# Optimization experiments

Measured on AMD Instinct MI355X. Metric: run time of the kernel, lower is better.

Reference implementation:

```python
import jax, jax.numpy as jnp
import numpy as np


def _pairwise_smooth_l1_sum(x):
    # x: [N, D]. All N^2 ordered pairs (i, j), including i == j (diff = 0),
    # matching torch's full index_select over [i for i ... for j ...].
    d = x[:, None, :] - x[None, :, :]            # [N, N, D]
    ad = jnp.abs(d)
    # SmoothL1 with beta = 1 (torch default): 0.5*d^2 if |d| < 1 else |d| - 0.5
    sl1 = jnp.where(ad < 1.0, 0.5 * d * d, ad - 0.5)
    return jnp.sum(sl1, axis=-1).reshape(-1)     # [N*N]


def setup_inputs() -> dict:
    key = jax.random.key(0)
    k1, k2 = jax.random.split(key)
    N, D = 512, 512
    teacher = jax.random.normal(k1, (N, D), dtype=jnp.float32)
    student = jax.random.normal(k2, (N, D), dtype=jnp.float32)
    return {"teacher": teacher, "student": student}


def reference(teacher, student):
    teacher_l2s = _pairwise_smooth_l1_sum(teacher)
    teacher_l2s = teacher_l2s / jnp.mean(teacher_l2s)
    student_l2s = _pairwise_smooth_l1_sum(student)
    student_l2s = student_l2s / jnp.mean(student_l2s)
    return jnp.sum(jnp.abs(teacher_l2s - student_l2s))
```

## Files before the change

kernel.cpp:

```cpp
#include <hip/hip_runtime.h>

#define N 512
#define D 512
#define TILE 32
#define DC 64
#define PAD 68

__device__ __forceinline__ void sl1(float& acc, float x, float y) {
    float d  = x - y;
    float ad = fabsf(d);
    float m  = fminf(ad, 1.0f);
    acc = fmaf(m, fmaf(2.0f, ad, -m), acc);
}

__global__ __launch_bounds__(64) void zero_kernel(float* sums, float* out) {
    if (threadIdx.x == 0) { sums[0] = 0.0f; sums[1] = 0.0f; out[0] = 0.0f; }
}

__global__ __launch_bounds__(256) void pair_sums_kernel(
    const float* __restrict__ Tm, const float* __restrict__ Sm,
    float* __restrict__ P, float* __restrict__ sums)
{
    const int mat = blockIdx.z;
    const float* __restrict__ X = mat ? Sm : Tm;
    float* __restrict__ Pm = P + (size_t)mat * (N * N);

    __shared__ float Xi[TILE][PAD];
    __shared__ float Xj[TILE][PAD];

    const int i0 = blockIdx.y * TILE;
    const int j0 = blockIdx.x * TILE;
    const int t  = threadIdx.x;
    const int tx = t & 15;
    const int ty = t >> 4;

    float a00 = 0.f, a01 = 0.f, a10 = 0.f, a11 = 0.f;

    for (int dc = 0; dc < D; dc += DC) {
        __syncthreads();
        #pragma unroll
        for (int k = 0; k < 2; ++k) {
            int idx = t + k * 256;
            int row = idx >> 4;
            int c4  = (idx & 15) * 4;
            *(float4*)&Xi[row][c4] = *(const float4*)&X[(size_t)(i0 + row) * D + dc + c4];
            *(float4*)&Xj[row][c4] = *(const float4*)&X[(size_t)(j0 + row) * D + dc + c4];
        }
        __syncthreads();
        #pragma unroll 4
        for (int d4 = 0; d4 < DC / 4; ++d4) {
            float4 p0 = *(const float4*)&Xi[ty][d4 * 4];
            float4 p1 = *(const float4*)&Xi[ty + 16][d4 * 4];
            float4 q0 = *(const float4*)&Xj[tx][d4 * 4];
            float4 q1 = *(const float4*)&Xj[tx + 16][d4 * 4];
            sl1(a00, p0.x, q0.x); sl1(a00, p0.y, q0.y); sl1(a00, p0.z, q0.z); sl1(a00, p0.w, q0.w);
            sl1(a01, p0.x, q1.x); sl1(a01, p0.y, q1.y); sl1(a01, p0.z, q1.z); sl1(a01, p0.w, q1.w);
            sl1(a10, p1.x, q0.x); sl1(a10, p1.y, q0.y); sl1(a10, p1.z, q0.z); sl1(a10, p1.w, q0.w);
            sl1(a11, p1.x, q1.x); sl1(a11, p1.y, q1.y); sl1(a11, p1.z, q1.z); sl1(a11, p1.w, q1.w);
        }
    }

    float s00 = 0.5f * a00, s01 = 0.5f * a01, s10 = 0.5f * a10, s11 = 0.5f * a11;
    Pm[(size_t)(i0 + ty     ) * N + (j0 + tx     )] = s00;
    Pm[(size_t)(i0 + ty     ) * N + (j0 + tx + 16)] = s01;
    Pm[(size_t)(i0 + ty + 16) * N + (j0 + tx     )] = s10;
    Pm[(size_t)(i0 + ty + 16) * N + (j0 + tx + 16)] = s11;

    float bs = s00 + s01 + s10 + s11;
    #pragma unroll
    for (int off = 32; off > 0; off >>= 1) bs += __shfl_down(bs, off, 64);
    __shared__ float wpart[4];
    if ((t & 63) == 0) wpart[t >> 6] = bs;
    __syncthreads();
    if (t == 0) atomicAdd(&sums[mat], wpart[0] + wpart[1] + wpart[2] + wpart[3]);
}

__global__ __launch_bounds__(256) void final_kernel(
    const float* __restrict__ P, const float* __restrict__ sums, float* __restrict__ out)
{
    const float NN = (float)(N * N);
    const float cT = NN / sums[0];
    const float cS = NN / sums[1];
    float local = 0.0f;
    for (int p = blockIdx.x * 256 + threadIdx.x; p < N * N; p += gridDim.x * 256) {
        local += fabsf(P[p] * cT - P[N * N + p] * cS);
    }
    #pragma unroll
    for (int off = 32; off > 0; off >>= 1) local += __shfl_down(local, off, 64);
    __shared__ float wpart[4];
    if ((threadIdx.x & 63) == 0) wpart[threadIdx.x >> 6] = local;
    __syncthreads();
    if (threadIdx.x == 0) atomicAdd(out, wpart[0] + wpart[1] + wpart[2] + wpart[3]);
}

extern "C" void kernel_launch(void* const* d_in, const int* in_sizes, int n_in,
                              void* d_out, int out_size, void* d_ws, size_t ws_size,
                              hipStream_t stream) {
    const float* teacher = (const float*)d_in[0];
    const float* student = (const float*)d_in[1];
    float* out  = (float*)d_out;
    float* P    = (float*)d_ws;
    float* sums = P + 2 * (size_t)N * N;

    zero_kernel<<<1, 64, 0, stream>>>(sums, out);
    dim3 grid(N / TILE, N / TILE, 2);
    pair_sums_kernel<<<grid, 256, 0, stream>>>(teacher, student, P, sums);
    final_kernel<<<128, 256, 0, stream>>>(P, sums, out);
}
```

Measured before the change: 100.8 us.

## Exploit pair symmetry with upper-triangle tiles and split-D atomic accumulation

The pair kernel now computes only upper-triangular 32x32 tiles (136 instead of 256) and splits the feature dimension into 8 slices, one per block. Each block atomically adds its partial sums into a pre-zeroed workspace. The final kernel reads only the upper triangle with float4 loads and doubles the total, with the mean sums rescaled to match. This roughly halves the arithmetic and raises parallelism, at the cost of global float atomics, a full-workspace memset each call, and a possible change in float summation order.

```diff
diff --git a/kernel.cpp b/kernel.cpp
--- a/kernel.cpp
+++ b/kernel.cpp
@@ -4,7 +4,10 @@
 #define D 512
 #define TILE 32
 #define DC 64
-#define PAD 68
+#define PITCH 68
+#define NT 16
+#define NTILES 136
+#define NSLICE 8
 
 __device__ __forceinline__ void sl1(float& acc, float x, float y) {
     float d  = x - y;
@@ -13,11 +16,7 @@
     acc = fmaf(m, fmaf(2.0f, ad, -m), acc);
 }
 
-__global__ __launch_bounds__(64) void zero_kernel(float* sums, float* out) {
-    if (threadIdx.x == 0) { sums[0] = 0.0f; sums[1] = 0.0f; out[0] = 0.0f; }
-}
-
-__global__ __launch_bounds__(256) void pair_sums_kernel(
+__global__ __launch_bounds__(256, 8) void pair_sums_kernel(
     const float* __restrict__ Tm, const float* __restrict__ Sm,
     float* __restrict__ P, float* __restrict__ sums)
 {
@@ -25,48 +24,53 @@
     const float* __restrict__ X = mat ? Sm : Tm;
     float* __restrict__ Pm = P + (size_t)mat * (N * N);
 
-    __shared__ float Xi[TILE][PAD];
-    __shared__ float Xj[TILE][PAD];
+    int rem = blockIdx.x, ti = 0;
+    while (rem >= NT - ti) { rem -= NT - ti; ++ti; }
+    const int tj = ti + rem;
+    const int i0 = ti * TILE, j0 = tj * TILE;
+    const int d0 = blockIdx.y * DC;
 
-    const int i0 = blockIdx.y * TILE;
-    const int j0 = blockIdx.x * TILE;
+    __shared__ float Xi[TILE][PITCH];
+    __shared__ float Xj[TILE][PITCH];
+
     const int t  = threadIdx.x;
     const int tx = t & 15;
     const int ty = t >> 4;
 
+    #pragma unroll
+    for (int kk = 0; kk < 2; ++kk) {
+        int idx = t + kk * 256;
+        int row = idx >> 4;
+        int c4  = (idx & 15) * 4;
+        *(float4*)&Xi[row][c4] = *(const float4*)&X[(size_t)(i0 + row) * D + d0 + c4];
+        *(float4*)&Xj[row][c4] = *(const float4*)&X[(size_t)(j0 + row) * D + d0 + c4];
+    }
+    __syncthreads();
+
     float a00 = 0.f, a01 = 0.f, a10 = 0.f, a11 = 0.f;
-
-    for (int dc = 0; dc < D; dc += DC) {
-        __syncthreads();
-        #pragma unroll
-        for (int k = 0; k < 2; ++k) {
-            int idx = t + k * 256;
-            int row = idx >> 4;
-            int c4  = (idx & 15) * 4;
-            *(float4*)&Xi[row][c4] = *(const float4*)&X[(size_t)(i0 + row) * D + dc + c4];
-            *(float4*)&Xj[row][c4] = *(const float4*)&X[(size_t)(j0 + row) * D + dc + c4];
-        }
-        __syncthreads();
-        #pragma unroll 4
-        for (int d4 = 0; d4 < DC / 4; ++d4) {
-            float4 p0 = *(const float4*)&Xi[ty][d4 * 4];
-            float4 p1 = *(const float4*)&Xi[ty + 16][d4 * 4];
-            float4 q0 = *(const float4*)&Xj[tx][d4 * 4];
-            float4 q1 = *(const float4*)&Xj[tx + 16][d4 * 4];
-            sl1(a00, p0.x, q0.x); sl1(a00, p0.y, q0.y); sl1(a00, p0.z, q0.z); sl1(a00, p0.w, q0.w);
-            sl1(a01, p0.x, q1.x); sl1(a01, p0.y, q1.y); sl1(a01, p0.z, q1.z); sl1(a01, p0.w, q1.w);
-            sl1(a10, p1.x, q0.x); sl1(a10, p1.y, q0.y); sl1(a10, p1.z, q0.z); sl1(a10, p1.w, q0.w);
-            sl1(a11, p1.x, q1.x); sl1(a11, p1.y, q1.y); sl1(a11, p1.z, q1.z); sl1(a11, p1.w, q1.w);
-        }
+    #pragma unroll 4
+    for (int d4 = 0; d4 < DC / 4; ++d4) {
+        float4 p0 = *(const float4*)&Xi[ty][d4 * 4];
+        float4 p1 = *(const float4*)&Xi[ty + 16][d4 * 4];
+        float4 q0 = *(const float4*)&Xj[tx][d4 * 4];
+        float4 q1 = *(const float4*)&Xj[tx + 16][d4 * 4];
+        sl1(a00, p0.x, q0.x); sl1(a00, p0.y, q0.y); sl1(a00, p0.z, q0.z); sl1(a00, p0.w, q0.w);
+        sl1(a01, p0.x, q1.x); sl1(a01, p0.y, q1.y); sl1(a01, p0.z, q1.z); sl1(a01, p0.w, q1.w);
+        sl1(a10, p1.x, q0.x); sl1(a10, p1.y, q0.y); sl1(a10, p1.z, q0.z); sl1(a10, p1.w, q0.w);
+        sl1(a11, p1.x, q1.x); sl1(a11, p1.y, q1.y); sl1(a11, p1.z, q1.z); sl1(a11, p1.w, q1.w);
     }
 
-    float s00 = 0.5f * a00, s01 = 0.5f * a01, s10 = 0.5f * a10, s11 = 0.5f * a11;
-    Pm[(size_t)(i0 + ty     ) * N + (j0 + tx     )] = s00;
-    Pm[(size_t)(i0 + ty     ) * N + (j0 + tx + 16)] = s01;
-    Pm[(size_t)(i0 + ty + 16) * N + (j0 + tx     )] = s10;
-    Pm[(size_t)(i0 + ty + 16) * N + (j0 + tx + 16)] = s11;
+    const bool diag = (ti == tj);
+    const bool w00 = !diag || (ty <= tx);
+    const bool w10 = !diag;
+    const float s00 = 0.5f * a00, s01 = 0.5f * a01, s10 = 0.5f * a10, s11 = 0.5f * a11;
 
-    float bs = s00 + s01 + s10 + s11;
+    float bs = 0.f;
+    if (w00) { atomicAdd(&Pm[(i0 + ty     ) * N + (j0 + tx     )], s00); bs += s00; }
+              { atomicAdd(&Pm[(i0 + ty     ) * N + (j0 + tx + 16)], s01); bs += s01; }
+    if (w10) { atomicAdd(&Pm[(i0 + ty + 16) * N + (j0 + tx     )], s10); bs += s10; }
+    if (w00) { atomicAdd(&Pm[(i0 + ty + 16) * N + (j0 + tx + 16)], s11); bs += s11; }
+
     #pragma unroll
     for (int off = 32; off > 0; off >>= 1) bs += __shfl_down(bs, off, 64);
     __shared__ float wpart[4];
@@ -78,19 +82,28 @@
 __global__ __launch_bounds__(256) void final_kernel(
     const float* __restrict__ P, const float* __restrict__ sums, float* __restrict__ out)
 {
-    const float NN = (float)(N * N);
-    const float cT = NN / sums[0];
-    const float cS = NN / sums[1];
+    const float NN = (float)N * (float)N;
+    const float cT = NN / (2.0f * sums[0]);
+    const float cS = NN / (2.0f * sums[1]);
     float local = 0.0f;
-    for (int p = blockIdx.x * 256 + threadIdx.x; p < N * N; p += gridDim.x * 256) {
-        local += fabsf(P[p] * cT - P[N * N + p] * cS);
+    const int nvec = N * N / 4;
+    for (int v = blockIdx.x * 256 + threadIdx.x; v < nvec; v += gridDim.x * 256) {
+        int i  = v >> 7;
+        int jb = (v & 127) * 4;
+        if (jb + 3 < i) continue;
+        float4 tq = ((const float4*)P)[v];
+        float4 sq = ((const float4*)(P + (size_t)N * N))[v];
+        if (jb + 0 >= i) local += fabsf(tq.x * cT - sq.x * cS);
+        if (jb + 1 >= i) local += fabsf(tq.y * cT - sq.y * cS);
+        if (jb + 2 >= i) local += fabsf(tq.z * cT - sq.z * cS);
+        if (jb + 3 >= i) local += fabsf(tq.w * cT - sq.w * cS);
     }
     #pragma unroll
     for (int off = 32; off > 0; off >>= 1) local += __shfl_down(local, off, 64);
     __shared__ float wpart[4];
     if ((threadIdx.x & 63) == 0) wpart[threadIdx.x >> 6] = local;
     __syncthreads();
-    if (threadIdx.x == 0) atomicAdd(out, wpart[0] + wpart[1] + wpart[2] + wpart[3]);
+    if (threadIdx.x == 0) atomicAdd(out, 2.0f * (wpart[0] + wpart[1] + wpart[2] + wpart[3]));
 }
 
 extern "C" void kernel_launch(void* const* d_in, const int* in_sizes, int n_in,
@@ -102,8 +115,10 @@
     float* P    = (float*)d_ws;
     float* sums = P + 2 * (size_t)N * N;
 
-    zero_kernel<<<1, 64, 0, stream>>>(sums, out);
-    dim3 grid(N / TILE, N / TILE, 2);
+    hipMemsetAsync(d_ws, 0, (2 * (size_t)N * N + 2) * sizeof(float), stream);
+    hipMemsetAsync(d_out, 0, sizeof(float), stream);
+
+    dim3 grid(NTILES, NSLICE, 2);
     pair_sums_kernel<<<grid, 256, 0, stream>>>(teacher, student, P, sums);
     final_kernel<<<128, 256, 0, stream>>>(P, sums, out);
 }
```

Result: faster. 97.52 us (-3.3%).
